# Kernel tuning notes

Hardware: AMD Instinct MI355X
Metric: run time of the kernel (lower is better)

The kernel has to match this reference:

```python
import jax, jax.numpy as jnp
import numpy as np

NUM_EXPERT = 8
IN_FEAT = 1024
OUT_FEAT = 1024
N_TOKENS = 8192


def setup_inputs() -> dict:
    key = jax.random.key(0)
    k_inp, k_gate, k_w = jax.random.split(key, 3)
    inp = jax.random.normal(k_inp, (N_TOKENS, IN_FEAT), dtype=jnp.float32)
    gate = jax.random.randint(k_gate, (N_TOKENS,), 0, NUM_EXPERT, dtype=jnp.int32)
    # FMoELinear weight: [num_expert, out_feat, in_feat], kaiming-uniform-like init
    bound = 1.0 / np.sqrt(IN_FEAT)
    weight = jax.random.uniform(
        k_w, (NUM_EXPERT, OUT_FEAT, IN_FEAT), dtype=jnp.float32,
        minval=-bound, maxval=bound)
    return {"inp": inp, "gate": gate, "weight": weight}


def reference(inp, gate, weight):
    # out[i] = weight[gate[i]] @ inp[i]  (top-1 MoE dispatch + grouped GEMM + combine)
    # Loop over the small fixed expert set via scan; each step does a masked
    # dense GEMM so only tokens routed to expert e contribute.
    n, _ = inp.shape
    num_expert, out_feat, _ = weight.shape

    def body(acc, ew):
        e, w_e = ew  # w_e: [out_feat, in_feat]
        mask = (gate == e).astype(inp.dtype)[:, None]  # [n, 1]
        acc = acc + (inp * mask) @ w_e.T               # [n, out_feat]
        return acc, None

    init = jnp.zeros((n, out_feat), dtype=inp.dtype)
    out, _ = jax.lax.scan(body, init, (jnp.arange(num_expert), weight))
    return out
```

## Files before the change

### kernel.cpp

```cpp
#include <hip/hip_runtime.h>
#include <hip/hip_bf16.h>

#define N_TOKENS 8192
#define IN_FEAT 1024
#define OUT_FEAT 1024
#define NUM_EXPERT 8

#define BM 128
#define BN 128
#define BK 32

typedef __bf16 bf16x8 __attribute__((ext_vector_type(8)));
typedef float f32x4 __attribute__((ext_vector_type(4)));

__device__ __forceinline__ unsigned int rne16(float x) {
    union { float f; unsigned int u; } c;
    c.f = x;
    unsigned int u = c.u;
    u += 0x7fffu + ((u >> 16) & 1u);
    return u >> 16;
}
__device__ __forceinline__ unsigned int pk2(float x, float y) {
    return rne16(x) | (rne16(y) << 16);
}

__device__ __forceinline__ void load_lds16(const void* g, void* l) {
    __builtin_amdgcn_global_load_lds(
        (const __attribute__((address_space(1))) unsigned int*)g,
        (__attribute__((address_space(3))) unsigned int*)l,
        16, 0, 0);
}


__global__ __launch_bounds__(256) void moe_hist(const int* __restrict__ gate,
                                                int* __restrict__ cnt) {
    __shared__ int lc[NUM_EXPERT];
    const int t = threadIdx.x;
    if (t < NUM_EXPERT) lc[t] = 0;
    __syncthreads();
    int g = gate[blockIdx.x * 256 + t];
    atomicAdd(&lc[g], 1);
    __syncthreads();
    if (t < NUM_EXPERT) atomicAdd(&cnt[t], lc[t]);
}

__global__ void moe_scan(const int* __restrict__ cnt, int* __restrict__ seg,
                         int* __restrict__ cur) {
    int s = 0;
    #pragma unroll
    for (int e = 0; e < NUM_EXPERT; ++e) { seg[e] = s; cur[e] = s; s += cnt[e]; }
    seg[NUM_EXPERT] = s;
}

__global__ __launch_bounds__(256) void moe_scatter(const int* __restrict__ gate,
                                                   int* __restrict__ cur,
                                                   int* __restrict__ perm) {
    const int t = threadIdx.x;
    const int lane = t & 63;
    const unsigned long long lt = (lane == 0) ? 0ull : (~0ull >> (64 - lane));
    const int i = blockIdx.x * 256 + t;
    int g = gate[i];
    #pragma unroll
    for (int e = 0; e < NUM_EXPERT; ++e) {
        unsigned long long m = __ballot(g == e);
        if (g == e) {
            int rank = __popcll(m & lt);
            int leader = (int)__ffsll((unsigned long long)m) - 1;
            int p0 = 0;
            if (rank == 0) p0 = atomicAdd(&cur[e], __popcll(m));
            p0 = __shfl(p0, leader);
            perm[p0 + rank] = i;
        }
    }
}

__global__ __launch_bounds__(256) void moe_prep(const float* __restrict__ inp,
                                                const float* __restrict__ weight,
                                                const int* __restrict__ perm,
                                                unsigned int* __restrict__ A2,
                                                unsigned int* __restrict__ W2) {
    const int bid = blockIdx.x;
    const int t = threadIdx.x;
    const int wave = t >> 6, lane = t & 63;
    const float* src;
    unsigned int* dst;
    if (bid < 2048) {
        int row = bid * 4 + wave;
        src = inp + perm[row] * IN_FEAT;
        dst = A2 + row * (IN_FEAT / 2);
    } else {
        int row = (bid - 2048) * 4 + wave;
        src = weight + row * IN_FEAT;
        dst = W2 + row * (IN_FEAT / 2);
    }
    #pragma unroll
    for (int j = 0; j < 4; ++j) {
        float4 v = *(const float4*)(src + j * 256 + lane * 4);
        uint2 o;
        o.x = pk2(v.x, v.y);
        o.y = pk2(v.z, v.w);
        *(uint2*)(dst + j * 128 + lane * 2) = o;
    }
}

__global__ __launch_bounds__(256, 4) void moe_gemm(
    const unsigned short* __restrict__ A2,
    const unsigned short* __restrict__ W2,
    const int* __restrict__ perm,
    const int* __restrict__ seg,
    float* __restrict__ out) {

    const int bid = blockIdx.x;
    const int e = bid & 7;
    const int ntile = (bid >> 3) & 7;
    const int mtile = bid >> 6;

    const int base = seg[e];
    const int cnt = seg[e + 1] - base;
    if (mtile * BM >= cnt) return;
    const int tbase = base + mtile * BM;
    int rows = cnt - mtile * BM; if (rows > BM) rows = BM;

    __shared__ __align__(16) unsigned short lA[2][BM * BK];
    __shared__ __align__(16) unsigned short lB[2][BN * BK];

    const int t = threadIdx.x;

    const int crow = t >> 2;
    const int p = (t & 3) ^ (crow & 3);
    int ar0 = tbase + crow;       if (ar0 > N_TOKENS - 1) ar0 = N_TOKENS - 1;
    int ar1 = tbase + 64 + crow;  if (ar1 > N_TOKENS - 1) ar1 = N_TOKENS - 1;
    const unsigned short* gA0 = A2 + ar0 * IN_FEAT + p * 8;
    const unsigned short* gA1 = A2 + ar1 * IN_FEAT + p * 8;
    const unsigned short* gB0 = W2 + e * (OUT_FEAT * IN_FEAT)
                                + (ntile * BN + crow) * IN_FEAT + p * 8;
    const unsigned short* gB1 = gB0 + 64 * IN_FEAT;
    const int dofs = t * 8;
    const int dofs2 = (t + 256) * 8;

    const int wave = t >> 6;
    const int lane = t & 63;
    const int wm = (wave & 1) << 6;
    const int wn = (wave >> 1) << 6;
    const int l15 = lane & 15;
    const int quad = lane >> 4;
    const int qx = quad ^ (l15 & 3);
    const int fofsA = (wm + l15) * BK + qx * 8;
    const int fofsB = (wn + l15) * BK + qx * 8;

    f32x4 acc[4][4];
    #pragma unroll
    for (int i = 0; i < 4; ++i)
        #pragma unroll
        for (int j = 0; j < 4; ++j)
            acc[i][j] = (f32x4)0.0f;

    load_lds16(gA0, &lA[0][dofs]);
    load_lds16(gA1, &lA[0][dofs2]);
    load_lds16(gB0, &lB[0][dofs]);
    load_lds16(gB1, &lB[0][dofs2]);

    #pragma unroll 1
    for (int kk = 0; kk < 16; ++kk) {
        const int k0 = kk * 64;

        __syncthreads();
        load_lds16(gA0 + k0 + 32, &lA[1][dofs]);
        load_lds16(gA1 + k0 + 32, &lA[1][dofs2]);
        load_lds16(gB0 + k0 + 32, &lB[1][dofs]);
        load_lds16(gB1 + k0 + 32, &lB[1][dofs2]);

        {
            bf16x8 af[4], bq[4];
            #pragma unroll
            for (int i = 0; i < 4; ++i)
                af[i] = *(const bf16x8*)&lA[0][fofsA + i * 16 * BK];
            #pragma unroll
            for (int j = 0; j < 4; ++j)
                bq[j] = *(const bf16x8*)&lB[0][fofsB + j * 16 * BK];
            #pragma unroll
            for (int i = 0; i < 4; ++i)
                #pragma unroll
                for (int j = 0; j < 4; ++j)
                    acc[i][j] = __builtin_amdgcn_mfma_f32_16x16x32_bf16(
                        af[i], bq[j], acc[i][j], 0, 0, 0);
        }

        __syncthreads();
        if (kk < 15) {
            load_lds16(gA0 + k0 + 64, &lA[0][dofs]);
            load_lds16(gA1 + k0 + 64, &lA[0][dofs2]);
            load_lds16(gB0 + k0 + 64, &lB[0][dofs]);
            load_lds16(gB1 + k0 + 64, &lB[0][dofs2]);
        }

        {
            bf16x8 af[4], bq[4];
            #pragma unroll
            for (int i = 0; i < 4; ++i)
                af[i] = *(const bf16x8*)&lA[1][fofsA + i * 16 * BK];
            #pragma unroll
            for (int j = 0; j < 4; ++j)
                bq[j] = *(const bf16x8*)&lB[1][fofsB + j * 16 * BK];
            #pragma unroll
            for (int i = 0; i < 4; ++i)
                #pragma unroll
                for (int j = 0; j < 4; ++j)
                    acc[i][j] = __builtin_amdgcn_mfma_f32_16x16x32_bf16(
                        af[i], bq[j], acc[i][j], 0, 0, 0);
        }
    }

    #pragma unroll
    for (int mi = 0; mi < 4; ++mi) {
        #pragma unroll
        for (int r = 0; r < 4; ++r) {
            int row = wm + mi * 16 + quad * 4 + r;
            if (row < rows) {
                int token = perm[tbase + row];
                float* op = out + token * OUT_FEAT + ntile * BN + wn;
                #pragma unroll
                for (int ni = 0; ni < 4; ++ni)
                    op[ni * 16 + l15] = acc[mi][ni][r];
            }
        }
    }
}

#define FLDSW 20
__global__ __launch_bounds__(256, 4) void moe_gemm_fb(
    const float* __restrict__ inp,
    const float* __restrict__ weight,
    const int* __restrict__ perm,
    const int* __restrict__ seg,
    float* __restrict__ out) {

    const int bid = blockIdx.x;
    const int mtile = bid >> 7;
    const int e = (bid >> 4) & 7;
    const int ntile = bid & 15;

    const int base = seg[e];
    const int cnt = seg[e + 1] - base;
    if (mtile * 128 >= cnt) return;

    __shared__ unsigned int lA[128 * FLDSW];
    __shared__ unsigned int lB[64 * FLDSW];
    __shared__ int rowids[128];

    const int t = threadIdx.x;
    if (t < 128) {
        int r = mtile * 128 + t;
        rowids[t] = (r < cnt) ? perm[base + r] : -1;
    }
    __syncthreads();

    const int srow = t >> 1;
    const int scol = (t & 1) << 4;
    const int tokA = rowids[srow];
    const bool aval = (tokA >= 0);
    const float* aptr = inp + (aval ? tokA : 0) * IN_FEAT + scol;
    const int sdstA = srow * FLDSW + (scol >> 1);
    const int browB = t >> 2;
    const int bcol = (t & 3) << 3;
    const float* bptr = weight + e * (OUT_FEAT * IN_FEAT)
                        + (ntile * 64 + browB) * IN_FEAT + bcol;
    const int sdstB = browB * FLDSW + (bcol >> 1);

    const int wave = t >> 6;
    const int lane = t & 63;
    const int wm = (wave & 1) << 6;
    const int wn = (wave >> 1) << 5;
    const int l15 = lane & 15;
    const int quad = lane >> 4;

    f32x4 acc[4][2];
    #pragma unroll
    for (int i = 0; i < 4; ++i)
        #pragma unroll
        for (int j = 0; j < 2; ++j)
            acc[i][j] = (f32x4)0.0f;

    float4 ra[4], rb[2];
    {
        const float4* ap = (const float4*)aptr;
        const float4* bp = (const float4*)bptr;
        #pragma unroll
        for (int i = 0; i < 4; ++i) ra[i] = ap[i];
        #pragma unroll
        for (int i = 0; i < 2; ++i) rb[i] = bp[i];
    }

    for (int k0 = 0; k0 < IN_FEAT; k0 += 32) {
        unsigned int ua[8], ub[4];
        #pragma unroll
        for (int i = 0; i < 4; ++i) {
            ua[2 * i]     = pk2(ra[i].x, ra[i].y);
            ua[2 * i + 1] = pk2(ra[i].z, ra[i].w);
        }
        #pragma unroll
        for (int i = 0; i < 2; ++i) {
            ub[2 * i]     = pk2(rb[i].x, rb[i].y);
            ub[2 * i + 1] = pk2(rb[i].z, rb[i].w);
        }
        if (!aval) {
            #pragma unroll
            for (int i = 0; i < 8; ++i) ua[i] = 0u;
        }

        __syncthreads();
        *(uint4*)&lA[sdstA]     = make_uint4(ua[0], ua[1], ua[2], ua[3]);
        *(uint4*)&lA[sdstA + 4] = make_uint4(ua[4], ua[5], ua[6], ua[7]);
        *(uint4*)&lB[sdstB]     = make_uint4(ub[0], ub[1], ub[2], ub[3]);
        __syncthreads();

        if (k0 + 32 < IN_FEAT) {
            const float4* ap = (const float4*)(aptr + k0 + 32);
            const float4* bp = (const float4*)(bptr + k0 + 32);
            #pragma unroll
            for (int i = 0; i < 4; ++i) ra[i] = ap[i];
            #pragma unroll
            for (int i = 0; i < 2; ++i) rb[i] = bp[i];
        }

        bf16x8 af[4], bq[2];
        #pragma unroll
        for (int i = 0; i < 4; ++i)
            af[i] = *(const bf16x8*)&lA[(wm + i * 16 + l15) * FLDSW + (quad << 2)];
        #pragma unroll
        for (int j = 0; j < 2; ++j)
            bq[j] = *(const bf16x8*)&lB[(wn + j * 16 + l15) * FLDSW + (quad << 2)];

        #pragma unroll
        for (int i = 0; i < 4; ++i)
            #pragma unroll
            for (int j = 0; j < 2; ++j)
                acc[i][j] = __builtin_amdgcn_mfma_f32_16x16x32_bf16(
                    af[i], bq[j], acc[i][j], 0, 0, 0);
    }

    #pragma unroll
    for (int mi = 0; mi < 4; ++mi) {
        #pragma unroll
        for (int r = 0; r < 4; ++r) {
            int row = wm + mi * 16 + quad * 4 + r;
            int token = rowids[row];
            if (token >= 0) {
                float* op = out + token * OUT_FEAT + ntile * 64 + wn;
                #pragma unroll
                for (int ni = 0; ni < 2; ++ni)
                    op[ni * 16 + l15] = acc[mi][ni][r];
            }
        }
    }
}

extern "C" void kernel_launch(void* const* d_in, const int* in_sizes, int n_in,
                              void* d_out, int out_size, void* d_ws, size_t ws_size,
                              hipStream_t stream) {
    const float* inp = (const float*)d_in[0];
    const int* gate = (const int*)d_in[1];
    const float* weight = (const float*)d_in[2];
    float* out = (float*)d_out;

    int* perm = (int*)d_ws;
    int* seg = perm + N_TOKENS;
    int* cnt = seg + 16;
    int* cur = cnt + 8;

    hipMemsetAsync(cnt, 0, 16 * sizeof(int), stream);
    moe_hist<<<N_TOKENS / 256, 256, 0, stream>>>(gate, cnt);
    moe_scan<<<1, 1, 0, stream>>>(cnt, seg, cur);
    moe_scatter<<<N_TOKENS / 256, 256, 0, stream>>>(gate, cur, perm);

    const size_t need = 65536 + 2ull * N_TOKENS * IN_FEAT * 2;
    if (ws_size >= need) {
        unsigned int* A2 = (unsigned int*)((char*)d_ws + 65536);
        unsigned int* W2 = A2 + (N_TOKENS * IN_FEAT / 2);
        moe_prep<<<4096, 256, 0, stream>>>(inp, weight, perm, A2, W2);
        moe_gemm<<<4096, 256, 0, stream>>>((const unsigned short*)A2,
                                           (const unsigned short*)W2,
                                           perm, seg, out);
    } else {
        moe_gemm_fb<<<8192, 256, 0, stream>>>(inp, weight, perm, seg, out);
    }
}
```

Measured before the change: 153.1 us.

## Fuse routing histogram, scan, scatter and bf16 conversion into two kernels

Replaces the memset, histogram, scan, scatter and prep launches with a single-block setup kernel that counts tokens per expert and writes segment offsets, then a combined kernel that scatters tokens and converts their rows to bf16 directly into permuted positions, alongside weight conversion. This removes several launches and the separate perm-dependent gather pass. Converted loads are widened to two float4 per lane. In exchange, the single-block histogram serialises over all tokens in one workgroup, and atomic ordering changes the permutation across runs.

```diff
diff --git a/kernel.cpp b/kernel.cpp
--- a/kernel.cpp
+++ b/kernel.cpp
@@ -31,75 +31,101 @@
         16, 0, 0);
 }
 
-
-__global__ __launch_bounds__(256) void moe_hist(const int* __restrict__ gate,
-                                                int* __restrict__ cnt) {
+__global__ __launch_bounds__(1024) void moe_setup(const int* __restrict__ gate,
+                                                  int* __restrict__ seg,
+                                                  int* __restrict__ cur) {
     __shared__ int lc[NUM_EXPERT];
     const int t = threadIdx.x;
+    const int lane = t & 63;
     if (t < NUM_EXPERT) lc[t] = 0;
     __syncthreads();
-    int g = gate[blockIdx.x * 256 + t];
-    atomicAdd(&lc[g], 1);
+    #pragma unroll
+    for (int i = 0; i < 8; ++i) {
+        int g = gate[t + i * 1024];
+        #pragma unroll
+        for (int e = 0; e < NUM_EXPERT; ++e) {
+            unsigned long long m = __ballot(g == e);
+            if (lane == 0 && m) atomicAdd(&lc[e], __popcll(m));
+        }
+    }
     __syncthreads();
-    if (t < NUM_EXPERT) atomicAdd(&cnt[t], lc[t]);
-}
-
-__global__ void moe_scan(const int* __restrict__ cnt, int* __restrict__ seg,
-                         int* __restrict__ cur) {
-    int s = 0;
-    #pragma unroll
-    for (int e = 0; e < NUM_EXPERT; ++e) { seg[e] = s; cur[e] = s; s += cnt[e]; }
-    seg[NUM_EXPERT] = s;
-}
-
-__global__ __launch_bounds__(256) void moe_scatter(const int* __restrict__ gate,
-                                                   int* __restrict__ cur,
-                                                   int* __restrict__ perm) {
+    if (t == 0) {
+        int s = 0;
+        #pragma unroll
+        for (int e = 0; e < NUM_EXPERT; ++e) { seg[e] = s; cur[e] = s; s += lc[e]; }
+        seg[NUM_EXPERT] = s;
+    }
+}
+
+__global__ __launch_bounds__(256) void moe_sp(const int* __restrict__ gate,
+                                              int* __restrict__ cur,
+                                              int* __restrict__ perm,
+                                              const float* __restrict__ inp,
+                                              const float* __restrict__ weight,
+                                              unsigned int* __restrict__ A2,
+                                              unsigned int* __restrict__ W2,
+                                              int doA) {
+    const int b = blockIdx.x;
     const int t = threadIdx.x;
     const int lane = t & 63;
-    const unsigned long long lt = (lane == 0) ? 0ull : (~0ull >> (64 - lane));
-    const int i = blockIdx.x * 256 + t;
-    int g = gate[i];
-    #pragma unroll
-    for (int e = 0; e < NUM_EXPERT; ++e) {
-        unsigned long long m = __ballot(g == e);
-        if (g == e) {
-            int rank = __popcll(m & lt);
-            int leader = (int)__ffsll((unsigned long long)m) - 1;
-            int p0 = 0;
-            if (rank == 0) p0 = atomicAdd(&cur[e], __popcll(m));
-            p0 = __shfl(p0, leader);
-            perm[p0 + rank] = i;
-        }
-    }
-}
-
-__global__ __launch_bounds__(256) void moe_prep(const float* __restrict__ inp,
-                                                const float* __restrict__ weight,
-                                                const int* __restrict__ perm,
-                                                unsigned int* __restrict__ A2,
-                                                unsigned int* __restrict__ W2) {
-    const int bid = blockIdx.x;
-    const int t = threadIdx.x;
-    const int wave = t >> 6, lane = t & 63;
-    const float* src;
-    unsigned int* dst;
-    if (bid < 2048) {
-        int row = bid * 4 + wave;
-        src = inp + perm[row] * IN_FEAT;
-        dst = A2 + row * (IN_FEAT / 2);
-    } else {
-        int row = (bid - 2048) * 4 + wave;
-        src = weight + row * IN_FEAT;
-        dst = W2 + row * (IN_FEAT / 2);
-    }
-    #pragma unroll
-    for (int j = 0; j < 4; ++j) {
-        float4 v = *(const float4*)(src + j * 256 + lane * 4);
-        uint2 o;
-        o.x = pk2(v.x, v.y);
-        o.y = pk2(v.z, v.w);
-        *(uint2*)(dst + j * 128 + lane * 2) = o;
+
+    if (b >= 256) {
+        const int row = (b - 256) * 4 + (t >> 6);
+        const float* src = weight + row * IN_FEAT;
+        unsigned int* dst = W2 + row * (IN_FEAT / 2);
+        #pragma unroll
+        for (int ps = 0; ps < 2; ++ps) {
+            float4 v0 = *(const float4*)(src + ps * 512 + lane * 8);
+            float4 v1 = *(const float4*)(src + ps * 512 + lane * 8 + 4);
+            uint4 o;
+            o.x = pk2(v0.x, v0.y); o.y = pk2(v0.z, v0.w);
+            o.z = pk2(v1.x, v1.y); o.w = pk2(v1.z, v1.w);
+            *(uint4*)(dst + ps * 256 + lane * 4) = o;
+        }
+        return;
+    }
+
+    __shared__ int lpos[32];
+    if (t < 32) {
+        const unsigned long long lt =
+            (lane == 0) ? 0ull : (~0ull >> (64 - lane));
+        const int i = b * 32 + t;
+        int g = gate[i];
+        #pragma unroll
+        for (int e = 0; e < NUM_EXPERT; ++e) {
+            unsigned long long m = __ballot(g == e);
+            if (g == e) {
+                int rank = __popcll(m & lt);
+                int leader = (int)__ffsll((unsigned long long)m) - 1;
+                int p0 = 0;
+                if (rank == 0) p0 = atomicAdd(&cur[e], __popcll(m));
+                p0 = __shfl(p0, leader);
+                int pos = p0 + rank;
+                perm[pos] = i;
+                lpos[t] = pos;
+            }
+        }
+    }
+    __syncthreads();
+    if (!doA) return;
+
+    const int w = t >> 6;
+    #pragma unroll
+    for (int j = 0; j < 8; ++j) {
+        const int idx = w * 8 + j;
+        const int tok = b * 32 + idx;
+        const int drow = lpos[idx];
+        const float* src = inp + tok * IN_FEAT;
+        unsigned int* dst = A2 + drow * (IN_FEAT / 2);
+        #pragma unroll
+        for (int ps = 0; ps < 2; ++ps) {
+            float4 v0 = *(const float4*)(src + ps * 512 + lane * 8);
+            float4 v1 = *(const float4*)(src + ps * 512 + lane * 8 + 4);
+            uint4 o;
+            o.x = pk2(v0.x, v0.y); o.y = pk2(v0.z, v0.w);
+            o.z = pk2(v1.x, v1.y); o.w = pk2(v1.z, v1.w);
+            *(uint4*)(dst + ps * 256 + lane * 4) = o;
+        }
     }
 }
 
@@ -365,19 +391,18 @@
 
     int* perm = (int*)d_ws;
     int* seg = perm + N_TOKENS;
-    int* cnt = seg + 16;
-    int* cur = cnt + 8;
-
-    hipMemsetAsync(cnt, 0, 16 * sizeof(int), stream);
-    moe_hist<<<N_TOKENS / 256, 256, 0, stream>>>(gate, cnt);
-    moe_scan<<<1, 1, 0, stream>>>(cnt, seg, cur);
-    moe_scatter<<<N_TOKENS / 256, 256, 0, stream>>>(gate, cur, perm);
+    int* cur = seg + 16;
 
     const size_t need = 65536 + 2ull * N_TOKENS * IN_FEAT * 2;
-    if (ws_size >= need) {
-        unsigned int* A2 = (unsigned int*)((char*)d_ws + 65536);
-        unsigned int* W2 = A2 + (N_TOKENS * IN_FEAT / 2);
-        moe_prep<<<4096, 256, 0, stream>>>(inp, weight, perm, A2, W2);
+    const int useBf16 = (ws_size >= need);
+    unsigned int* A2 = (unsigned int*)((char*)d_ws + 65536);
+    unsigned int* W2 = A2 + (N_TOKENS * IN_FEAT / 2);
+
+    moe_setup<<<1, 1024, 0, stream>>>(gate, seg, cur);
+    moe_sp<<<useBf16 ? 2304 : 256, 256, 0, stream>>>(
+        gate, cur, perm, inp, weight, A2, W2, useBf16);
+
+    if (useBf16) {
         moe_gemm<<<4096, 256, 0, stream>>>((const unsigned short*)A2,
                                            (const unsigned short*)W2,
                                            perm, seg, out);
```

Measured after the change: 161.0 us. 5.2% more time.
